# Performance work log

Measured on AMD Instinct MI355X. Metric: run time of the kernel, lower is better.

## Reference

```python
import jax, jax.numpy as jnp
import numpy as np

H = 2048        # hidden_size
E = 64          # num_experts
TOPK = 4        # top_k_experts
EPS = 1e-6      # rms_norm_eps
SW = 1024       # sliding_window
NEG = jnp.finfo(jnp.float32).min


def setup_inputs() -> dict:
    key = jax.random.key(0)
    k1, k2, k3, k4, k5 = jax.random.split(key, 5)
    B, S = 2, 4096
    x = jax.random.normal(k1, (B, S, H), jnp.float32)
    # 1-based document ids packed contiguously; 0 = padding
    packed_seq_ids = jnp.sort(jax.random.randint(k2, (B, S), 0, 5), axis=-1)
    # 0 = text, 1/2 = vision tokens
    mm_token_type_ids = jax.random.randint(k3, (B, S), 0, 3)
    scale = jax.random.uniform(k4, (H,), jnp.float32, 0.5, 1.5)
    proj_w = jax.random.normal(k5, (E, H), jnp.float32) * 0.02
    return dict(x=x, packed_seq_ids=packed_seq_ids,
                mm_token_type_ids=mm_token_type_ids, scale=scale, proj_w=proj_w)


def _vision_group_ids(mm):
    # per-image-block ids for vision tokens, -1 for text/padding
    is_v = (mm == 1) | (mm == 2)
    is_prev = jnp.concatenate([jnp.zeros_like(is_v[:, :1]), is_v[:, :-1]], axis=-1)
    starts = is_v & ~is_prev
    gid = jnp.cumsum(starts.astype(jnp.int32), axis=1) - 1
    return jnp.where(is_v, gid, -1)


def _build_masks(packed, mm, sliding_window):
    B, S = packed.shape
    pos = jnp.arange(S)
    causal = pos[None, :, None] >= pos[None, None, :]          # [1,S,S] kv<=q
    valid_q = packed[:, :, None] > 0
    valid_kv = packed[:, None, :] > 0
    same_doc = (packed[:, :, None] == packed[:, None, :]) & valid_q & valid_kv
    full = same_doc & causal                                   # [B,S,S]
    sliding = full & ((pos[None, :, None] - pos[None, None, :]) < sliding_window)
    gid = _vision_group_ids(mm)
    same_vg = (gid[:, :, None] == gid[:, None, :]) & (gid[:, :, None] >= 0)
    sliding = (sliding | same_vg) & same_doc
    # additive format, [B,1,S,S]
    full_add = jnp.where(full[:, None], jnp.float32(0.0), NEG)
    sliding_add = jnp.where(sliding[:, None], jnp.float32(0.0), NEG)
    return full_add, sliding_add


def _gate(x, scale, proj_w):
    # Gemma4Gate: RMSNorm(no scale) -> H**-0.5 -> learnable scale -> linear
    #             -> softmax -> top-k -> renormalize
    xf = x.reshape(-1, H)                                      # [N,H]
    xn = xf * jax.lax.rsqrt(jnp.mean(xf * xf, axis=-1, keepdims=True) + EPS)
    xn = xn * (H ** -0.5) * scale
    logits = jnp.einsum('nh,eh->ne', xn, proj_w)               # [N,E]
    probs = jax.nn.softmax(logits, axis=-1)
    weights, indices = jax.lax.top_k(probs, TOPK)              # [N,K]
    weights = weights / jnp.maximum(jnp.sum(weights, axis=-1, keepdims=True), 1e-20)
    return weights, indices


def reference(x, packed_seq_ids, mm_token_type_ids, scale, proj_w):
    full_mask, sliding_mask = _build_masks(packed_seq_ids, mm_token_type_ids, SW)
    weights, indices = _gate(x, scale, proj_w)
    return full_mask, sliding_mask, weights, indices
```

## Files before the change

### kernel.cpp

```cpp
#include <hip/hip_runtime.h>
#include <math.h>

#define S 4096
#define HH 2048
#define NE 64
#define SW 1024
#define MASKED 0xFBFFu

typedef unsigned short u16;
typedef unsigned int u32;

__device__ __align__(16) int g_gid[2 * S];
__device__ __align__(16) float g_pw2[NE * HH];

__device__ __forceinline__ float h2f(u32 lo16) {
    union { u16 u; _Float16 h; } v; v.u = (u16)lo16; return (float)v.h;
}
__device__ __forceinline__ u16 f2h(float f) {
    union { u16 u; _Float16 h; } v; v.h = (_Float16)f; return v.u;
}
__device__ __forceinline__ void u4_to_f8(uint4 v, float* o) {
    o[0] = h2f(v.x & 0xFFFFu); o[1] = h2f(v.x >> 16);
    o[2] = h2f(v.y & 0xFFFFu); o[3] = h2f(v.y >> 16);
    o[4] = h2f(v.z & 0xFFFFu); o[5] = h2f(v.z >> 16);
    o[6] = h2f(v.w & 0xFFFFu); o[7] = h2f(v.w >> 16);
}

__global__ __launch_bounds__(256) void pre_kernel(const int* __restrict__ mm,
                                                  const u16* __restrict__ proj_w) {
    const int blk = blockIdx.x;
    const int t = threadIdx.x;
    if (blk < 2) {
        __shared__ int ts[256];
        const int* m = mm + blk * S;
        const int base_pos = t * 16;
        int vals[16];
#pragma unroll
        for (int i = 0; i < 16; i++) vals[i] = m[base_pos + i];
        bool prevv = false;
        if (base_pos > 0) {
            int pv = m[base_pos - 1];
            prevv = (pv == 1) || (pv == 2);
        }
        int cnt = 0;
        {
            bool pv = prevv;
#pragma unroll
            for (int i = 0; i < 16; i++) {
                bool is = (vals[i] == 1) || (vals[i] == 2);
                cnt += (is && !pv) ? 1 : 0;
                pv = is;
            }
        }
        ts[t] = cnt;
        __syncthreads();
        for (int off = 1; off < 256; off <<= 1) {
            int add = (t >= off) ? ts[t - off] : 0;
            __syncthreads();
            ts[t] += add;
            __syncthreads();
        }
        int base = ts[t] - cnt;
        {
            bool pv = prevv;
            int run = base;
#pragma unroll
            for (int i = 0; i < 16; i++) {
                bool is = (vals[i] == 1) || (vals[i] == 2);
                run += (is && !pv) ? 1 : 0;
                g_gid[blk * S + base_pos + i] = is ? (run - 1) : -1;
                pv = is;
            }
        }
    } else {
        int idx = (blk - 2) * 256 + t;
        int e = idx >> 11;
        int h = idx & 2047;
        g_pw2[(h >> 2) * 256 + e * 4 + (h & 3)] = h2f((u32)proj_w[idx]);
    }
}

__global__ __launch_bounds__(256) void fused_kernel(
    const u16* __restrict__ x, const u16* __restrict__ scale,
    const int* __restrict__ packed,
    u16* __restrict__ full_out, u16* __restrict__ slid_out,
    u16* __restrict__ w_out, u16* __restrict__ i_out) {

    __shared__ float factor[16];
    __shared__ float xs[16][132];
    __shared__ float part[4][16][65];

    const int t = threadIdx.x;

    if (blockIdx.x >= 512) {
        const int tid = (blockIdx.x - 512) * 256 + t;
        const int kc = tid & 511;
        const int q = (tid >> 9) & 4095;
        const int b = tid >> 21;
        const int k0 = kc * 8;

        const int pq = packed[b * S + q];
        const int gq = g_gid[b * S + q];
        const int4 pk0 = *(const int4*)(packed + b * S + k0);
        const int4 pk1 = *(const int4*)(packed + b * S + k0 + 4);
        const int4 gk0 = *(const int4*)(g_gid + b * S + k0);
        const int4 gk1 = *(const int4*)(g_gid + b * S + k0 + 4);

        int pkj[8] = {pk0.x, pk0.y, pk0.z, pk0.w, pk1.x, pk1.y, pk1.z, pk1.w};
        int gkj[8] = {gk0.x, gk0.y, gk0.z, gk0.w, gk1.x, gk1.y, gk1.z, gk1.w};
        u32 fm[8], sm[8];
#pragma unroll
        for (int j = 0; j < 8; j++) {
            int k = k0 + j;
            bool sd = (pq > 0) && (pkj[j] == pq);
            bool fl = sd && (q >= k);
            bool sl = ((fl && ((q - k) < SW)) || ((gkj[j] == gq) && (gq >= 0))) && sd;
            fm[j] = fl ? 0u : MASKED;
            sm[j] = sl ? 0u : MASKED;
        }
        uint4 f4, s4;
        f4.x = fm[0] | (fm[1] << 16); f4.y = fm[2] | (fm[3] << 16);
        f4.z = fm[4] | (fm[5] << 16); f4.w = fm[6] | (fm[7] << 16);
        s4.x = sm[0] | (sm[1] << 16); s4.y = sm[2] | (sm[3] << 16);
        s4.z = sm[4] | (sm[5] << 16); s4.w = sm[6] | (sm[7] << 16);

        size_t off = (size_t)b * ((size_t)S * S) + (size_t)q * S + k0;
        *(uint4*)(full_out + off) = f4;
        *(uint4*)(slid_out + off) = s4;
        return;
    }

    const int w = t >> 6;
    const int l = t & 63;
    const int tok0 = blockIdx.x * 16;

    for (int tt = w; tt < 16; tt += 4) {
        const uint4* xp = (const uint4*)(x + (size_t)(tok0 + tt) * HH);
        float ss = 0.0f;
#pragma unroll
        for (int j = 0; j < 4; j++) {
            float o[8];
            u4_to_f8(xp[l + 64 * j], o);
#pragma unroll
            for (int i = 0; i < 8; i++) ss += o[i] * o[i];
        }
        for (int off = 32; off >= 1; off >>= 1) ss += __shfl_xor(ss, off);
        if (l == 0)
            factor[tt] = rsqrtf(ss * (1.0f / 2048.0f) + 1e-6f) * 0.022097086912079608f;
    }
    __syncthreads();

    const int g = l & 15;
    const int ts = l >> 4;
    float acc[4][4];
#pragma unroll
    for (int a = 0; a < 4; a++)
#pragma unroll
        for (int bb = 0; bb < 4; bb++) acc[a][bb] = 0.0f;

    const int stok = t >> 4;
    const int sh = (t & 15) * 8;
    const u16* xrow = x + (size_t)(tok0 + stok) * HH + sh;

    uint4 xv_p = *(const uint4*)(xrow);
    uint4 sv_p = *(const uint4*)(scale + sh);

    for (int ch = 0; ch < 16; ch++) {
        __syncthreads();
        {
            float xo[8], so[8];
            u4_to_f8(xv_p, xo);
            u4_to_f8(sv_p, so);
            float fac = factor[stok];
            float4 a, b;
            a.x = xo[0] * fac * so[0]; a.y = xo[1] * fac * so[1];
            a.z = xo[2] * fac * so[2]; a.w = xo[3] * fac * so[3];
            b.x = xo[4] * fac * so[4]; b.y = xo[5] * fac * so[5];
            b.z = xo[6] * fac * so[6]; b.w = xo[7] * fac * so[7];
            *(float4*)&xs[stok][sh] = a;
            *(float4*)&xs[stok][sh + 4] = b;
        }
        __syncthreads();
        if (ch < 15) {
            xv_p = *(const uint4*)(xrow + (ch + 1) * 128);
            sv_p = *(const uint4*)(scale + (ch + 1) * 128 + sh);
        }

        const float* pwb = g_pw2 + (size_t)(ch * 32 + w * 8) * 256 + g * 16;
#pragma unroll
        for (int i = 0; i < 8; i++) {
            float4 p[4];
#pragma unroll
            for (int ej = 0; ej < 4; ej++)
                p[ej] = *(const float4*)(pwb + (size_t)i * 256 + ej * 4);
#pragma unroll
            for (int tk = 0; tk < 4; tk++) {
                float4 xv = *(const float4*)&xs[4 * ts + tk][w * 32 + i * 4];
#pragma unroll
                for (int ej = 0; ej < 4; ej++)
                    acc[tk][ej] += p[ej].x * xv.x + p[ej].y * xv.y +
                                   p[ej].z * xv.z + p[ej].w * xv.w;
            }
        }
    }

#pragma unroll
    for (int tk = 0; tk < 4; tk++)
#pragma unroll
        for (int ej = 0; ej < 4; ej++)
            part[w][4 * ts + tk][4 * g + ej] = acc[tk][ej];
    __syncthreads();

    {
        int tok = t >> 4;
        int eg = t & 15;
        float lg[4];
#pragma unroll
        for (int j = 0; j < 4; j++) {
            int e = eg * 4 + j;
            lg[j] = part[0][tok][e] + part[1][tok][e] + part[2][tok][e] + part[3][tok][e];
        }
        *(float4*)&xs[tok][eg * 4] = make_float4(lg[0], lg[1], lg[2], lg[3]);
    }
    __syncthreads();

    if (t < 16) {
        unsigned long long used = 0ull;
        float bv[4];
        int bi[4];
#pragma unroll
        for (int p = 0; p < 4; p++) {
            float best = -INFINITY;
            int besti = 0;
            for (int e = 0; e < NE; e++) {
                if (used & (1ull << e)) continue;
                float v = xs[t][e];
                if (v > best) { best = v; besti = e; }
            }
            used |= 1ull << besti;
            bv[p] = best;
            bi[p] = besti;
        }
        float ww[4];
        float ssum = 0.0f;
#pragma unroll
        for (int p = 0; p < 4; p++) { ww[p] = expf(bv[p] - bv[0]); ssum += ww[p]; }
        int n = tok0 + t;
#pragma unroll
        for (int p = 0; p < 4; p++) {
            w_out[n * 4 + p] = f2h(ww[p] / ssum);
            i_out[n * 4 + p] = f2h((float)bi[p]);
        }
    }
}

extern "C" void kernel_launch(void* const* d_in, const int* in_sizes, int n_in,
                              void* d_out, int out_size, void* d_ws, size_t ws_size,
                              hipStream_t stream) {
    const u16* x = (const u16*)d_in[0];
    const int* packed = (const int*)d_in[1];
    const int* mm = (const int*)d_in[2];
    const u16* scale = (const u16*)d_in[3];
    const u16* proj_w = (const u16*)d_in[4];

    u16* out = (u16*)d_out;
    u16* full_out = out;
    u16* slid_out = out + 33554432;
    u16* w_out = out + 67108864;
    u16* i_out = out + 67141632;

    pre_kernel<<<514, 256, 0, stream>>>(mm, proj_w);
    fused_kernel<<<512 + 16384, 256, 0, stream>>>(x, scale, packed,
                                                  full_out, slid_out, w_out, i_out);
    (void)in_sizes; (void)n_in; (void)out_size; (void)d_ws; (void)ws_size;
}
```

Baseline: 361.7 us.

## Halve gate tokens per block and double-buffer the normalized-x tile

The gate part of the fused kernel now handles 8 tokens per block instead of 16, which doubles the gate grid to 1024 blocks, and it adds launch_bounds with a minimum of 4 blocks per unit. The shared xs tile is double-buffered, so each chunk needs one barrier instead of two and the next chunk's scaled activations are staged while the current one is consumed. This aims to spread the gate GEMV over more CUs and cut barrier stalls. The cost is that each block reloads the projection weights for half as many tokens, so the weight traffic from L2 doubles.

```diff
diff --git a/kernel.cpp b/kernel.cpp
--- a/kernel.cpp
+++ b/kernel.cpp
@@ -6,6 +6,7 @@
 #define NE 64
 #define SW 1024
 #define MASKED 0xFBFFu
+#define GB 1024
 
 typedef unsigned short u16;
 typedef unsigned int u32;
@@ -24,6 +25,10 @@
     o[2] = h2f(v.y & 0xFFFFu); o[3] = h2f(v.y >> 16);
     o[4] = h2f(v.z & 0xFFFFu); o[5] = h2f(v.z >> 16);
     o[6] = h2f(v.w & 0xFFFFu); o[7] = h2f(v.w >> 16);
+}
+__device__ __forceinline__ void u2_to_f4(uint2 v, float* o) {
+    o[0] = h2f(v.x & 0xFFFFu); o[1] = h2f(v.x >> 16);
+    o[2] = h2f(v.y & 0xFFFFu); o[3] = h2f(v.y >> 16);
 }
 
 __global__ __launch_bounds__(256) void pre_kernel(const int* __restrict__ mm,
@@ -80,20 +85,20 @@
     }
 }
 
-__global__ __launch_bounds__(256) void fused_kernel(
+__global__ __launch_bounds__(256, 4) void fused_kernel(
     const u16* __restrict__ x, const u16* __restrict__ scale,
     const int* __restrict__ packed,
     u16* __restrict__ full_out, u16* __restrict__ slid_out,
     u16* __restrict__ w_out, u16* __restrict__ i_out) {
 
-    __shared__ float factor[16];
-    __shared__ float xs[16][132];
-    __shared__ float part[4][16][65];
+    __shared__ float factor[8];
+    __shared__ float xs[2][8][132];
+    __shared__ float part[4][8][68];
 
     const int t = threadIdx.x;
 
-    if (blockIdx.x >= 512) {
-        const int tid = (blockIdx.x - 512) * 256 + t;
+    if (blockIdx.x >= GB) {
+        const int tid = (blockIdx.x - GB) * 256 + t;
         const int kc = tid & 511;
         const int q = (tid >> 9) & 4095;
         const int b = tid >> 21;
@@ -132,9 +137,9 @@
 
     const int w = t >> 6;
     const int l = t & 63;
-    const int tok0 = blockIdx.x * 16;
-
-    for (int tt = w; tt < 16; tt += 4) {
+    const int tok0 = blockIdx.x * 8;
+
+    for (int tt = w; tt < 8; tt += 4) {
         const uint4* xp = (const uint4*)(x + (size_t)(tok0 + tt) * HH);
         float ss = 0.0f;
 #pragma unroll
@@ -152,38 +157,42 @@
 
     const int g = l & 15;
     const int ts = l >> 4;
-    float acc[4][4];
-#pragma unroll
-    for (int a = 0; a < 4; a++)
+    float acc[2][4];
+#pragma unroll
+    for (int a = 0; a < 2; a++)
 #pragma unroll
         for (int bb = 0; bb < 4; bb++) acc[a][bb] = 0.0f;
 
-    const int stok = t >> 4;
-    const int sh = (t & 15) * 8;
+    const int stok = t >> 5;
+    const int sh = (t & 31) * 4;
     const u16* xrow = x + (size_t)(tok0 + stok) * HH + sh;
-
-    uint4 xv_p = *(const uint4*)(xrow);
-    uint4 sv_p = *(const uint4*)(scale + sh);
+    const float fac = factor[stok];
+
+    {
+        uint2 xv0 = *(const uint2*)(xrow);
+        uint2 sv0 = *(const uint2*)(scale + sh);
+        float xo[4], so[4];
+        u2_to_f4(xv0, xo); u2_to_f4(sv0, so);
+        *(float4*)&xs[0][stok][sh] = make_float4(
+            xo[0] * fac * so[0], xo[1] * fac * so[1],
+            xo[2] * fac * so[2], xo[3] * fac * so[3]);
+    }
+    uint2 xv_p = *(const uint2*)(xrow + 128);
+    uint2 sv_p = *(const uint2*)(scale + 128 + sh);
+    __syncthreads();
 
     for (int ch = 0; ch < 16; ch++) {
-        __syncthreads();
-        {
-            float xo[8], so[8];
-            u4_to_f8(xv_p, xo);
-            u4_to_f8(sv_p, so);
-            float fac = factor[stok];
-            float4 a, b;
-            a.x = xo[0] * fac * so[0]; a.y = xo[1] * fac * so[1];
-            a.z = xo[2] * fac * so[2]; a.w = xo[3] * fac * so[3];
-            b.x = xo[4] * fac * so[4]; b.y = xo[5] * fac * so[5];
-            b.z = xo[6] * fac * so[6]; b.w = xo[7] * fac * so[7];
-            *(float4*)&xs[stok][sh] = a;
-            *(float4*)&xs[stok][sh + 4] = b;
-        }
-        __syncthreads();
+        const int cur = ch & 1, nxt = cur ^ 1;
         if (ch < 15) {
-            xv_p = *(const uint4*)(xrow + (ch + 1) * 128);
-            sv_p = *(const uint4*)(scale + (ch + 1) * 128 + sh);
+            float xo[4], so[4];
+            u2_to_f4(xv_p, xo); u2_to_f4(sv_p, so);
+            *(float4*)&xs[nxt][stok][sh] = make_float4(
+                xo[0] * fac * so[0], xo[1] * fac * so[1],
+                xo[2] * fac * so[2], xo[3] * fac * so[3]);
+        }
+        if (ch < 14) {
+            xv_p = *(const uint2*)(xrow + (ch + 2) * 128);
+            sv_p = *(const uint2*)(scale + (ch + 2) * 128 + sh);
         }
 
         const float* pwb = g_pw2 + (size_t)(ch * 32 + w * 8) * 256 + g * 16;
@@ -194,24 +203,24 @@
             for (int ej = 0; ej < 4; ej++)
                 p[ej] = *(const float4*)(pwb + (size_t)i * 256 + ej * 4);
 #pragma unroll
-            for (int tk = 0; tk < 4; tk++) {
-                float4 xv = *(const float4*)&xs[4 * ts + tk][w * 32 + i * 4];
+            for (int tk = 0; tk < 2; tk++) {
+                float4 xv = *(const float4*)&xs[cur][2 * ts + tk][w * 32 + i * 4];
 #pragma unroll
                 for (int ej = 0; ej < 4; ej++)
                     acc[tk][ej] += p[ej].x * xv.x + p[ej].y * xv.y +
                                    p[ej].z * xv.z + p[ej].w * xv.w;
             }
         }
-    }
-
-#pragma unroll
-    for (int tk = 0; tk < 4; tk++)
-#pragma unroll
-        for (int ej = 0; ej < 4; ej++)
-            part[w][4 * ts + tk][4 * g + ej] = acc[tk][ej];
-    __syncthreads();
-
-    {
+        __syncthreads();
+    }
+
+#pragma unroll
+    for (int tk = 0; tk < 2; tk++)
+        *(float4*)&part[w][2 * ts + tk][4 * g] =
+            make_float4(acc[tk][0], acc[tk][1], acc[tk][2], acc[tk][3]);
+    __syncthreads();
+
+    if (t < 128) {
         int tok = t >> 4;
         int eg = t & 15;
         float lg[4];
@@ -220,11 +229,11 @@
             int e = eg * 4 + j;
             lg[j] = part[0][tok][e] + part[1][tok][e] + part[2][tok][e] + part[3][tok][e];
         }
-        *(float4*)&xs[tok][eg * 4] = make_float4(lg[0], lg[1], lg[2], lg[3]);
-    }
-    __syncthreads();
-
-    if (t < 16) {
+        *(float4*)&xs[0][tok][eg * 4] = make_float4(lg[0], lg[1], lg[2], lg[3]);
+    }
+    __syncthreads();
+
+    if (t < 8) {
         unsigned long long used = 0ull;
         float bv[4];
         int bi[4];
@@ -234,7 +243,7 @@
             int besti = 0;
             for (int e = 0; e < NE; e++) {
                 if (used & (1ull << e)) continue;
-                float v = xs[t][e];
+                float v = xs[0][t][e];
                 if (v > best) { best = v; besti = e; }
             }
             used |= 1ull << besti;
@@ -270,7 +279,7 @@
     u16* i_out = out + 67141632;
 
     pre_kernel<<<514, 256, 0, stream>>>(mm, proj_w);
-    fused_kernel<<<512 + 16384, 256, 0, stream>>>(x, scale, packed,
-                                                  full_out, slid_out, w_out, i_out);
+    fused_kernel<<<GB + 16384, 256, 0, stream>>>(x, scale, packed,
+                                                 full_out, slid_out, w_out, i_out);
     (void)in_sizes; (void)n_in; (void)out_size; (void)d_ws; (void)ws_size;
 }
```

Measured after the change: 447.7 us. 1.24x slower.
